# Kernel optimization log

Measured on AMD Instinct MI355X. Metric: run time of the kernel, lower is better.

The kernel has to match this reference:

```python
import jax, jax.numpy as jnp
import numpy as np

G = 64          # voxel grid side
N_IN = 150000   # input points
N_OUT = 150000  # output points
K = 3           # cubic kernel size
CIN = 32
FOUT = 64


def _make_cloud(rng, n):
    flat = rng.permutation(G ** 3)[:n]
    x = flat % G
    y = (flat // G) % G
    z = flat // (G * G)
    pos = np.stack([x, y, z], axis=-1).astype(np.float32) + 0.5  # voxel centers
    return flat, pos


def setup_inputs() -> dict:
    rng = np.random.default_rng(0)
    flat_in, inp_pos = _make_cloud(rng, N_IN)
    _, out_pos = _make_cloud(np.random.default_rng(1), N_OUT)

    # Fixed-radius (Linf, r = K*voxel*0.51 = 1.53) search on the grid ==
    # 3x3x3 voxel neighborhood lookup. Build dense voxel -> point-index map.
    grid = np.full(G ** 3, -1, dtype=np.int64)
    grid[flat_in] = np.arange(N_IN)
    offs = np.stack(np.meshgrid(*([np.arange(-1, 2)] * 3), indexing='ij'), -1).reshape(-1, 3)  # [27,3]
    out_vox = (out_pos - 0.5).astype(np.int64)              # [M,3]
    nb = out_vox[:, None, :] + offs[None, :, :]             # [M,27,3]
    inb = ((nb >= 0) & (nb < G)).all(-1)                    # [M,27]
    flat = nb[..., 0] + G * nb[..., 1] + G * G * nb[..., 2]
    flat = np.where(inb, flat, 0)
    found = grid[flat]
    mask = inb & (found >= 0)
    nbr_idx = np.where(mask, found, 0).astype(np.int32)

    key = jax.random.key(0)
    k1, k2, k3, k4, k5 = jax.random.split(key, 5)
    return {
        'inp_features': jax.random.normal(k1, (N_IN, CIN), jnp.float32),
        'inp_positions': jnp.asarray(inp_pos),
        'out_positions': jnp.asarray(out_pos),
        'voxel_size': jnp.asarray(1.0, jnp.float32),
        'inp_importance': jax.random.uniform(k2, (N_IN,), jnp.float32),
        'kernel': jax.random.uniform(k3, (K, K, K, CIN, FOUT), jnp.float32, -0.05, 0.05),
        'bias': jnp.zeros((FOUT,), jnp.float32) + 0.01 * jax.random.normal(k4, (FOUT,)),
        'neighbor_index': jnp.asarray(nbr_idx),
        'neighbor_mask': jnp.asarray(mask),
    }


def _sparse_conv(inp_features, inp_positions, out_positions, voxel_size,
                 inp_importance, kernel, bias, neighbor_index, neighbor_mask):
    # offset = 0 (odd kernel). extent = kernel_size * voxel_size.
    extent = K * voxel_size
    nbr_pos = inp_positions[neighbor_index]                  # [M,Kn,3]
    rel = nbr_pos - out_positions[:, None, :]                # [M,Kn,3]
    # identity coordinate mapping: normalize to [-1,1] over the extent
    n = 2.0 * rel / extent
    # align_corners=False mapping to filter coords, + offset (=0)
    fcoord = (n * 0.5 + 0.5) * K - 0.5                        # [M,Kn,3] (x,y,z)
    idx = jnp.clip(jnp.round(fcoord).astype(jnp.int32), 0, K - 1)
    # kernel is indexed [z,y,x,cin,cout]; positions are [x,y,z]
    flat_cell = idx[..., 2] * (K * K) + idx[..., 1] * K + idx[..., 0]   # [M,Kn]
    onehot = jax.nn.one_hot(flat_cell, K ** 3, dtype=inp_features.dtype)  # [M,Kn,27]
    w = (inp_importance[neighbor_index] * neighbor_mask.astype(inp_features.dtype))  # [M,Kn]
    feat = inp_features[neighbor_index] * w[..., None]       # [M,Kn,Cin]
    # accumulate neighbor features into their kernel cell, then contract with kernel
    cellfeat = jnp.einsum('mko,mkc->moc', onehot, feat)      # [M,27,Cin]
    wflat = kernel.reshape(K ** 3, CIN, FOUT)
    out = jnp.einsum('moc,ocf->mf', cellfeat, wflat)         # [M,F]
    return out + bias


def reference(inp_features, inp_positions, out_positions, voxel_size,
              inp_importance, kernel, bias, neighbor_index, neighbor_mask):
    return _sparse_conv(inp_features, inp_positions, out_positions, voxel_size,
                        inp_importance, kernel, bias, neighbor_index, neighbor_mask)
```

## Files before the change

### kernel.cpp

```cpp
#include <hip/hip_runtime.h>
#include <hip/hip_bf16.h>

#define CELLS 27
#define CIN   32
#define FOUT  64
#define M_OUT 150000
#define N_INP 150000
#define ZROW  N_INP
#define PPW   32
#define NWAVE ((M_OUT + PPW - 1) / PPW)
#define NBLK  ((NWAVE + 3) / 4)
#define WT_BYTES (CELLS * CIN * FOUT * 2)
#define FB_ROWS  (N_INP + 1)
#define FB_BYTES (FB_ROWS * CIN * 2)

typedef __attribute__((ext_vector_type(4))) float f32x4;
typedef __attribute__((ext_vector_type(8))) short bf16x8;

__device__ __forceinline__ short f2bf(float x) {
    union { __hip_bfloat16 h; short s; } u;
    u.h = __float2bfloat16(x);
    return u.s;
}

__global__ __launch_bounds__(256) void prep_w_kernel(const float* __restrict__ W,
                                                     unsigned short* __restrict__ Wt) {
    int t = blockIdx.x * 256 + threadIdx.x;
    if (t >= CELLS * CIN * FOUT) return;
    int cell = t >> 11;
    int rem  = t & 2047;
    int cin  = rem >> 6;
    int fout = rem & 63;
    Wt[cell * 2048 + fout * 32 + cin] = (unsigned short)f2bf(W[t]);
}

__global__ __launch_bounds__(256) void prep_feat_kernel(const float* __restrict__ feat,
                                                        const float* __restrict__ imp,
                                                        unsigned short* __restrict__ fb) {
    int t = blockIdx.x * 256 + threadIdx.x;
    if (t >= FB_ROWS * 4) return;
    int i = t >> 2, c = t & 3;
    bf16x8 o = {0, 0, 0, 0, 0, 0, 0, 0};
    if (i < N_INP) {
        float w = imp[i];
        const float* fp = feat + (size_t)i * CIN + c * 8;
        f32x4 f0 = *(const f32x4*)fp;
        f32x4 f1 = *(const f32x4*)(fp + 4);
        o[0] = f2bf(f0.x * w); o[1] = f2bf(f0.y * w);
        o[2] = f2bf(f0.z * w); o[3] = f2bf(f0.w * w);
        o[4] = f2bf(f1.x * w); o[5] = f2bf(f1.y * w);
        o[6] = f2bf(f1.z * w); o[7] = f2bf(f1.w * w);
    }
    *(bf16x8*)(fb + (size_t)i * CIN + c * 8) = o;
}

__global__ __launch_bounds__(256) void conv32_kernel(
        const float* __restrict__ opos,
        const float* __restrict__ ipos,
        const int*   __restrict__ nbr,
        const unsigned short* __restrict__ Wt,
        const unsigned short* __restrict__ fb,
        const float* __restrict__ bias,
        float* __restrict__ out) {
    __shared__ int s_idx[4][CELLS * PPW];
    __shared__ int s_vox[4][PPW];

    const int wid  = threadIdx.x >> 6;
    const int lane = threadIdx.x & 63;
    const int wave = blockIdx.x * 4 + wid;
    const int m0   = wave * PPW;

    const int vx0 = (int)ipos[0];
    const int vy0 = (int)ipos[1];
    const int vz0 = (int)ipos[2];

    if (lane < PPW) {
        int m = m0 + lane;
        int vp = -1;
        if (m < M_OUT) {
            int vx = (int)opos[m * 3 + 0];
            int vy = (int)opos[m * 3 + 1];
            int vz = (int)opos[m * 3 + 2];
            vp = (vx + 1) | ((vy + 1) << 8) | ((vz + 1) << 16);
        }
        s_vox[wid][lane] = vp;
    }
    __syncthreads();

    for (int it = 0; it < (CELLS * PPW + 63) / 64; ++it) {
        int e = it * 64 + lane;
        if (e < CELLS * PPW) {
            int p = e / CELLS;
            int k = e - p * CELLS;
            int m = m0 + p;
            int id = (m < M_OUT) ? nbr[m * CELLS + k] : 0;
            int ox = k / 9, oy = (k / 3) % 3, oz = k % 3;
            int tgt = (vx0 - ox + 2) | ((vy0 - oy + 2) << 8) | ((vz0 - oz + 2) << 16);
            bool valid = (id != 0) | (s_vox[wid][p] == tgt);
            s_idx[wid][k * PPW + p] = valid ? id : ZROW;
        }
    }
    __syncthreads();

    const int g = lane >> 4;
    const int r = lane & 15;

    f32x4 acc[8];
#pragma unroll
    for (int i = 0; i < 8; ++i) acc[i] = (f32x4){0.f, 0.f, 0.f, 0.f};

#pragma unroll
    for (int k = 0; k < CELLS; ++k) {
        const int cell = (k % 3) * 9 + ((k / 3) % 3) * 3 + (k / 9);
        int i0 = s_idx[wid][k * PPW + r];
        int i1 = s_idx[wid][k * PPW + 16 + r];
        bf16x8 a0 = *(const bf16x8*)(fb + (size_t)i0 * CIN + g * 8);
        bf16x8 a1 = *(const bf16x8*)(fb + (size_t)i1 * CIN + g * 8);
        const unsigned short* wb = Wt + cell * (CIN * FOUT) + r * CIN + g * 8;
        bf16x8 b0 = *(const bf16x8*)(wb);
        bf16x8 b1 = *(const bf16x8*)(wb + 16 * CIN);
        bf16x8 b2 = *(const bf16x8*)(wb + 32 * CIN);
        bf16x8 b3 = *(const bf16x8*)(wb + 48 * CIN);
        acc[0] = __builtin_amdgcn_mfma_f32_16x16x32_bf16(a0, b0, acc[0], 0, 0, 0);
        acc[1] = __builtin_amdgcn_mfma_f32_16x16x32_bf16(a0, b1, acc[1], 0, 0, 0);
        acc[2] = __builtin_amdgcn_mfma_f32_16x16x32_bf16(a0, b2, acc[2], 0, 0, 0);
        acc[3] = __builtin_amdgcn_mfma_f32_16x16x32_bf16(a0, b3, acc[3], 0, 0, 0);
        acc[4] = __builtin_amdgcn_mfma_f32_16x16x32_bf16(a1, b0, acc[4], 0, 0, 0);
        acc[5] = __builtin_amdgcn_mfma_f32_16x16x32_bf16(a1, b1, acc[5], 0, 0, 0);
        acc[6] = __builtin_amdgcn_mfma_f32_16x16x32_bf16(a1, b2, acc[6], 0, 0, 0);
        acc[7] = __builtin_amdgcn_mfma_f32_16x16x32_bf16(a1, b3, acc[7], 0, 0, 0);
    }

    float bb0 = bias[r], bb1 = bias[16 + r], bb2 = bias[32 + r], bb3 = bias[48 + r];
#pragma unroll
    for (int frag = 0; frag < 2; ++frag) {
        int base = m0 + frag * 16 + 4 * g;
#pragma unroll
        for (int j = 0; j < 4; ++j) {
            int m = base + j;
            if (m < M_OUT) {
                float* op = out + (size_t)m * FOUT + r;
                op[0]  = acc[frag * 4 + 0][j] + bb0;
                op[16] = acc[frag * 4 + 1][j] + bb1;
                op[32] = acc[frag * 4 + 2][j] + bb2;
                op[48] = acc[frag * 4 + 3][j] + bb3;
            }
        }
    }
}

__global__ __launch_bounds__(256, 4) void sparse_conv_fallback(
        const float* __restrict__ feat,
        const float* __restrict__ inp_pos,
        const float* __restrict__ out_pos,
        const float* __restrict__ importance,
        const float* __restrict__ bias,
        const int*   __restrict__ nbr,
        const unsigned short* __restrict__ Wt,
        float* __restrict__ out) {
    __shared__ int   s_idx[4][CELLS * 16];
    __shared__ float s_w  [4][CELLS * 16];

    const int wid  = threadIdx.x >> 6;
    const int lane = threadIdx.x & 63;
    int wave_g = blockIdx.x * 4 + wid;
    if (wave_g >= (M_OUT / 16)) wave_g = (M_OUT / 16) - 1;
    const int m0 = wave_g * 16;

    const int vx0 = (int)inp_pos[0];
    const int vy0 = (int)inp_pos[1];
    const int vz0 = (int)inp_pos[2];

    for (int it = 0; it < 7; ++it) {
        int e = it * 64 + lane;
        if (e < CELLS * 16) {
            int r = e / CELLS;
            int k = e - r * CELLS;
            int m = m0 + r;
            int idx = nbr[m * CELLS + k];
            bool valid = (idx != 0);
            if (!valid) {
                int ox = k / 9 - 1;
                int oy = (k / 3) % 3 - 1;
                int oz = k % 3 - 1;
                valid = (((int)out_pos[m * 3 + 0] + ox) == vx0) &
                        (((int)out_pos[m * 3 + 1] + oy) == vy0) &
                        (((int)out_pos[m * 3 + 2] + oz) == vz0);
            }
            float w = valid ? importance[idx] : 0.0f;
            s_idx[wid][k * 16 + r] = idx;
            s_w  [wid][k * 16 + r] = w;
        }
    }
    __syncthreads();

    const int g = lane >> 4;
    const int r = lane & 15;

    f32x4 acc0 = {0.f, 0.f, 0.f, 0.f};
    f32x4 acc1 = {0.f, 0.f, 0.f, 0.f};
    f32x4 acc2 = {0.f, 0.f, 0.f, 0.f};
    f32x4 acc3 = {0.f, 0.f, 0.f, 0.f};

#pragma unroll
    for (int k = 0; k < CELLS; ++k) {
        const int cell = (k % 3) * 9 + ((k / 3) % 3) * 3 + (k / 9);
        int   idx = s_idx[wid][k * 16 + r];
        float w   = s_w  [wid][k * 16 + r];
        if (__any(w != 0.0f)) {
            const float* fp = feat + (size_t)idx * CIN + g * 8;
            f32x4 f0 = *(const f32x4*)(fp);
            f32x4 f1 = *(const f32x4*)(fp + 4);
            bf16x8 a;
            a[0] = f2bf(f0.x * w); a[1] = f2bf(f0.y * w);
            a[2] = f2bf(f0.z * w); a[3] = f2bf(f0.w * w);
            a[4] = f2bf(f1.x * w); a[5] = f2bf(f1.y * w);
            a[6] = f2bf(f1.z * w); a[7] = f2bf(f1.w * w);
            const unsigned short* wb = Wt + cell * 2048 + r * 32 + g * 8;
            bf16x8 b0 = *(const bf16x8*)(wb);
            bf16x8 b1 = *(const bf16x8*)(wb + 512);
            bf16x8 b2 = *(const bf16x8*)(wb + 1024);
            bf16x8 b3 = *(const bf16x8*)(wb + 1536);
            acc0 = __builtin_amdgcn_mfma_f32_16x16x32_bf16(a, b0, acc0, 0, 0, 0);
            acc1 = __builtin_amdgcn_mfma_f32_16x16x32_bf16(a, b1, acc1, 0, 0, 0);
            acc2 = __builtin_amdgcn_mfma_f32_16x16x32_bf16(a, b2, acc2, 0, 0, 0);
            acc3 = __builtin_amdgcn_mfma_f32_16x16x32_bf16(a, b3, acc3, 0, 0, 0);
        }
    }

    float bb0 = bias[r], bb1 = bias[16 + r], bb2 = bias[32 + r], bb3 = bias[48 + r];
    const int row0 = m0 + 4 * g;
#pragma unroll
    for (int j = 0; j < 4; ++j) {
        float* op = out + (size_t)(row0 + j) * FOUT + r;
        op[0]  = acc0[j] + bb0;
        op[16] = acc1[j] + bb1;
        op[32] = acc2[j] + bb2;
        op[48] = acc3[j] + bb3;
    }
}

extern "C" void kernel_launch(void* const* d_in, const int* in_sizes, int n_in,
                              void* d_out, int out_size, void* d_ws, size_t ws_size,
                              hipStream_t stream) {
    const float* feat = (const float*)d_in[0];
    const float* ipos = (const float*)d_in[1];
    const float* opos = (const float*)d_in[2];
    const float* imp  = (const float*)d_in[4];
    const float* W    = (const float*)d_in[5];
    const float* bias = (const float*)d_in[6];
    const int*   nbr  = (const int*)d_in[7];
    unsigned short* Wt = (unsigned short*)d_ws;
    float* out = (float*)d_out;

    hipLaunchKernelGGL(prep_w_kernel, dim3((CELLS * CIN * FOUT + 255) / 256), dim3(256),
                       0, stream, W, Wt);

    if (ws_size >= (size_t)WT_BYTES + (size_t)FB_BYTES) {
        unsigned short* fb = (unsigned short*)((char*)d_ws + WT_BYTES);
        hipLaunchKernelGGL(prep_feat_kernel, dim3((FB_ROWS * 4 + 255) / 256), dim3(256),
                           0, stream, feat, imp, fb);
        hipLaunchKernelGGL(conv32_kernel, dim3(NBLK), dim3(256), 0, stream,
                           opos, ipos, nbr, Wt, fb, bias, out);
    } else {
        int blocks = (M_OUT / 16 + 3) / 4;
        hipLaunchKernelGGL(sparse_conv_fallback, dim3(blocks), dim3(256), 0, stream,
                           feat, ipos, opos, imp, bias, nbr, Wt, out);
    }
}
```

Baseline: 179.1 us.

## Merge prep kernels and double-buffer gathers in the conv MFMA loop

Fuses the weight and feature prep kernels into one launch, removing a kernel launch. In the conv kernel, the shared-memory index table is transposed to point-major with padding to 28, and the A/B operand loads are software-pipelined two cells ahead, so global gathers overlap the MFMA work. The fallback path and the workspace-size check are removed, which assumes the workspace is always large enough. The prefetch buffers also increase register pressure.

Result: no change. 180.7 us (+0.9%).

```diff
diff --git a/kernel.cpp b/kernel.cpp
--- a/kernel.cpp
+++ b/kernel.cpp
@@ -10,7 +10,8 @@
 #define PPW   32
 #define NWAVE ((M_OUT + PPW - 1) / PPW)
 #define NBLK  ((NWAVE + 3) / 4)
-#define WT_BYTES (CELLS * CIN * FOUT * 2)
+#define WT_ELEMS (CELLS * CIN * FOUT)
+#define WT_BYTES (WT_ELEMS * 2)
 #define FB_ROWS  (N_INP + 1)
 #define FB_BYTES (FB_ROWS * CIN * 2)
 
@@ -23,36 +24,39 @@
     return u.s;
 }
 
-__global__ __launch_bounds__(256) void prep_w_kernel(const float* __restrict__ W,
-                                                     unsigned short* __restrict__ Wt) {
+__global__ __launch_bounds__(256) void prep_kernel(const float* __restrict__ W,
+                                                   const float* __restrict__ feat,
+                                                   const float* __restrict__ imp,
+                                                   unsigned short* __restrict__ Wt,
+                                                   unsigned short* __restrict__ fb) {
     int t = blockIdx.x * 256 + threadIdx.x;
-    if (t >= CELLS * CIN * FOUT) return;
-    int cell = t >> 11;
-    int rem  = t & 2047;
-    int cin  = rem >> 6;
-    int fout = rem & 63;
-    Wt[cell * 2048 + fout * 32 + cin] = (unsigned short)f2bf(W[t]);
+    if (t < FB_ROWS * 4) {
+        int i = t >> 2, c = t & 3;
+        bf16x8 o = {0, 0, 0, 0, 0, 0, 0, 0};
+        if (i < N_INP) {
+            float w = imp[i];
+            const float* fp = feat + (size_t)i * CIN + c * 8;
+            f32x4 f0 = *(const f32x4*)fp;
+            f32x4 f1 = *(const f32x4*)(fp + 4);
+            o[0] = f2bf(f0.x * w); o[1] = f2bf(f0.y * w);
+            o[2] = f2bf(f0.z * w); o[3] = f2bf(f0.w * w);
+            o[4] = f2bf(f1.x * w); o[5] = f2bf(f1.y * w);
+            o[6] = f2bf(f1.z * w); o[7] = f2bf(f1.w * w);
+        }
+        *(bf16x8*)(fb + (size_t)i * CIN + c * 8) = o;
+    } else {
+        int u = t - FB_ROWS * 4;
+        if (u < WT_ELEMS) {
+            int cell = u >> 11;
+            int rem  = u & 2047;
+            int cin  = rem >> 6;
+            int fout = rem & 63;
+            Wt[cell * 2048 + fout * 32 + cin] = (unsigned short)f2bf(W[u]);
+        }
+    }
 }
 
-__global__ __launch_bounds__(256) void prep_feat_kernel(const float* __restrict__ feat,
-                                                        const float* __restrict__ imp,
-                                                        unsigned short* __restrict__ fb) {
-    int t = blockIdx.x * 256 + threadIdx.x;
-    if (t >= FB_ROWS * 4) return;
-    int i = t >> 2, c = t & 3;
-    bf16x8 o = {0, 0, 0, 0, 0, 0, 0, 0};
-    if (i < N_INP) {
-        float w = imp[i];
-        const float* fp = feat + (size_t)i * CIN + c * 8;
-        f32x4 f0 = *(const f32x4*)fp;
-        f32x4 f1 = *(const f32x4*)(fp + 4);
-        o[0] = f2bf(f0.x * w); o[1] = f2bf(f0.y * w);
-        o[2] = f2bf(f0.z * w); o[3] = f2bf(f0.w * w);
-        o[4] = f2bf(f1.x * w); o[5] = f2bf(f1.y * w);
-        o[6] = f2bf(f1.z * w); o[7] = f2bf(f1.w * w);
-    }
-    *(bf16x8*)(fb + (size_t)i * CIN + c * 8) = o;
-}
+#define CELL_OF(k) (((k) % 3) * 9 + (((k) / 3) % 3) * 3 + ((k) / 9))
 
 __global__ __launch_bounds__(256) void conv32_kernel(
         const float* __restrict__ opos,
@@ -62,7 +66,7 @@
         const unsigned short* __restrict__ fb,
         const float* __restrict__ bias,
         float* __restrict__ out) {
-    __shared__ int s_idx[4][CELLS * PPW];
+    __shared__ int s_idx[4][PPW][28];
     __shared__ int s_vox[4][PPW];
 
     const int wid  = threadIdx.x >> 6;
@@ -78,16 +82,15 @@
         int m = m0 + lane;
         int vp = -1;
         if (m < M_OUT) {
-            int vx = (int)opos[m * 3 + 0];
-            int vy = (int)opos[m * 3 + 1];
-            int vz = (int)opos[m * 3 + 2];
-            vp = (vx + 1) | ((vy + 1) << 8) | ((vz + 1) << 16);
+            vp = ((int)opos[m * 3 + 0] + 1) |
+                 (((int)opos[m * 3 + 1] + 1) << 8) |
+                 (((int)opos[m * 3 + 2] + 1) << 16);
         }
         s_vox[wid][lane] = vp;
     }
     __syncthreads();
 
-    for (int it = 0; it < (CELLS * PPW + 63) / 64; ++it) {
+    for (int it = 0; it < 14; ++it) {
         int e = it * 64 + lane;
         if (e < CELLS * PPW) {
             int p = e / CELLS;
@@ -97,7 +100,7 @@
             int ox = k / 9, oy = (k / 3) % 3, oz = k % 3;
             int tgt = (vx0 - ox + 2) | ((vy0 - oy + 2) << 8) | ((vz0 - oz + 2) << 16);
             bool valid = (id != 0) | (s_vox[wid][p] == tgt);
-            s_idx[wid][k * PPW + p] = valid ? id : ZROW;
+            s_idx[wid][p][k] = valid ? id : ZROW;
         }
     }
     __syncthreads();
@@ -105,30 +108,54 @@
     const int g = lane >> 4;
     const int r = lane & 15;
 
+    const unsigned short* fbg = fb + g * 8;
+    const unsigned short* wb0 = Wt + r * CIN + g * 8;
+    const int* idxr0 = &s_idx[wid][r][0];
+    const int* idxr1 = &s_idx[wid][16 + r][0];
+
     f32x4 acc[8];
 #pragma unroll
     for (int i = 0; i < 8; ++i) acc[i] = (f32x4){0.f, 0.f, 0.f, 0.f};
 
+    int    pi0[2], pi1[2];
+    bf16x8 pa0[2], pa1[2];
+    bf16x8 pb[2][4];
+
+    {
+        int a0 = idxr0[0], a1 = idxr1[0];
+        int b0 = idxr0[1], b1 = idxr1[1];
+        pa0[0] = *(const bf16x8*)(fbg + (size_t)a0 * CIN);
+        pa1[0] = *(const bf16x8*)(fbg + (size_t)a1 * CIN);
+        pa0[1] = *(const bf16x8*)(fbg + (size_t)b0 * CIN);
+        pa1[1] = *(const bf16x8*)(fbg + (size_t)b1 * CIN);
+#pragma unroll
+        for (int t = 0; t < 4; ++t) {
+            pb[0][t] = *(const bf16x8*)(wb0 + CELL_OF(0) * (CIN * FOUT) + t * 16 * CIN);
+            pb[1][t] = *(const bf16x8*)(wb0 + CELL_OF(1) * (CIN * FOUT) + t * 16 * CIN);
+        }
+        pi0[0] = idxr0[2]; pi1[0] = idxr1[2];
+        pi0[1] = idxr0[3]; pi1[1] = idxr1[3];
+    }
+
 #pragma unroll
     for (int k = 0; k < CELLS; ++k) {
-        const int cell = (k % 3) * 9 + ((k / 3) % 3) * 3 + (k / 9);
-        int i0 = s_idx[wid][k * PPW + r];
-        int i1 = s_idx[wid][k * PPW + 16 + r];
-        bf16x8 a0 = *(const bf16x8*)(fb + (size_t)i0 * CIN + g * 8);
-        bf16x8 a1 = *(const bf16x8*)(fb + (size_t)i1 * CIN + g * 8);
-        const unsigned short* wb = Wt + cell * (CIN * FOUT) + r * CIN + g * 8;
-        bf16x8 b0 = *(const bf16x8*)(wb);
-        bf16x8 b1 = *(const bf16x8*)(wb + 16 * CIN);
-        bf16x8 b2 = *(const bf16x8*)(wb + 32 * CIN);
-        bf16x8 b3 = *(const bf16x8*)(wb + 48 * CIN);
-        acc[0] = __builtin_amdgcn_mfma_f32_16x16x32_bf16(a0, b0, acc[0], 0, 0, 0);
-        acc[1] = __builtin_amdgcn_mfma_f32_16x16x32_bf16(a0, b1, acc[1], 0, 0, 0);
-        acc[2] = __builtin_amdgcn_mfma_f32_16x16x32_bf16(a0, b2, acc[2], 0, 0, 0);
-        acc[3] = __builtin_amdgcn_mfma_f32_16x16x32_bf16(a0, b3, acc[3], 0, 0, 0);
-        acc[4] = __builtin_amdgcn_mfma_f32_16x16x32_bf16(a1, b0, acc[4], 0, 0, 0);
-        acc[5] = __builtin_amdgcn_mfma_f32_16x16x32_bf16(a1, b1, acc[5], 0, 0, 0);
-        acc[6] = __builtin_amdgcn_mfma_f32_16x16x32_bf16(a1, b2, acc[6], 0, 0, 0);
-        acc[7] = __builtin_amdgcn_mfma_f32_16x16x32_bf16(a1, b3, acc[7], 0, 0, 0);
+        const int s = k & 1;
+#pragma unroll
+        for (int t = 0; t < 4; ++t) {
+            acc[t]     = __builtin_amdgcn_mfma_f32_16x16x32_bf16(pa0[s], pb[s][t], acc[t],     0, 0, 0);
+            acc[4 + t] = __builtin_amdgcn_mfma_f32_16x16x32_bf16(pa1[s], pb[s][t], acc[4 + t], 0, 0, 0);
+        }
+        if (k + 2 < CELLS) {
+            pa0[s] = *(const bf16x8*)(fbg + (size_t)pi0[s] * CIN);
+            pa1[s] = *(const bf16x8*)(fbg + (size_t)pi1[s] * CIN);
+#pragma unroll
+            for (int t = 0; t < 4; ++t)
+                pb[s][t] = *(const bf16x8*)(wb0 + CELL_OF(k + 2) * (CIN * FOUT) + t * 16 * CIN);
+            if (k + 4 < CELLS) {
+                pi0[s] = idxr0[k + 4];
+                pi1[s] = idxr1[k + 4];
+            }
+        }
     }
 
     float bb0 = bias[r], bb1 = bias[16 + r], bb2 = bias[32 + r], bb3 = bias[48 + r];
@@ -149,97 +176,6 @@
     }
 }
 
-__global__ __launch_bounds__(256, 4) void sparse_conv_fallback(
-        const float* __restrict__ feat,
-        const float* __restrict__ inp_pos,
-        const float* __restrict__ out_pos,
-        const float* __restrict__ importance,
-        const float* __restrict__ bias,
-        const int*   __restrict__ nbr,
-        const unsigned short* __restrict__ Wt,
-        float* __restrict__ out) {
-    __shared__ int   s_idx[4][CELLS * 16];
-    __shared__ float s_w  [4][CELLS * 16];
-
-    const int wid  = threadIdx.x >> 6;
-    const int lane = threadIdx.x & 63;
-    int wave_g = blockIdx.x * 4 + wid;
-    if (wave_g >= (M_OUT / 16)) wave_g = (M_OUT / 16) - 1;
-    const int m0 = wave_g * 16;
-
-    const int vx0 = (int)inp_pos[0];
-    const int vy0 = (int)inp_pos[1];
-    const int vz0 = (int)inp_pos[2];
-
-    for (int it = 0; it < 7; ++it) {
-        int e = it * 64 + lane;
-        if (e < CELLS * 16) {
-            int r = e / CELLS;
-            int k = e - r * CELLS;
-            int m = m0 + r;
-            int idx = nbr[m * CELLS + k];
-            bool valid = (idx != 0);
-            if (!valid) {
-                int ox = k / 9 - 1;
-                int oy = (k / 3) % 3 - 1;
-                int oz = k % 3 - 1;
-                valid = (((int)out_pos[m * 3 + 0] + ox) == vx0) &
-                        (((int)out_pos[m * 3 + 1] + oy) == vy0) &
-                        (((int)out_pos[m * 3 + 2] + oz) == vz0);
-            }
-            float w = valid ? importance[idx] : 0.0f;
-            s_idx[wid][k * 16 + r] = idx;
-            s_w  [wid][k * 16 + r] = w;
-        }
-    }
-    __syncthreads();
-
-    const int g = lane >> 4;
-    const int r = lane & 15;
-
-    f32x4 acc0 = {0.f, 0.f, 0.f, 0.f};
-    f32x4 acc1 = {0.f, 0.f, 0.f, 0.f};
-    f32x4 acc2 = {0.f, 0.f, 0.f, 0.f};
-    f32x4 acc3 = {0.f, 0.f, 0.f, 0.f};
-
-#pragma unroll
-    for (int k = 0; k < CELLS; ++k) {
-        const int cell = (k % 3) * 9 + ((k / 3) % 3) * 3 + (k / 9);
-        int   idx = s_idx[wid][k * 16 + r];
-        float w   = s_w  [wid][k * 16 + r];
-        if (__any(w != 0.0f)) {
-            const float* fp = feat + (size_t)idx * CIN + g * 8;
-            f32x4 f0 = *(const f32x4*)(fp);
-            f32x4 f1 = *(const f32x4*)(fp + 4);
-            bf16x8 a;
-            a[0] = f2bf(f0.x * w); a[1] = f2bf(f0.y * w);
-            a[2] = f2bf(f0.z * w); a[3] = f2bf(f0.w * w);
-            a[4] = f2bf(f1.x * w); a[5] = f2bf(f1.y * w);
-            a[6] = f2bf(f1.z * w); a[7] = f2bf(f1.w * w);
-            const unsigned short* wb = Wt + cell * 2048 + r * 32 + g * 8;
-            bf16x8 b0 = *(const bf16x8*)(wb);
-            bf16x8 b1 = *(const bf16x8*)(wb + 512);
-            bf16x8 b2 = *(const bf16x8*)(wb + 1024);
-            bf16x8 b3 = *(const bf16x8*)(wb + 1536);
-            acc0 = __builtin_amdgcn_mfma_f32_16x16x32_bf16(a, b0, acc0, 0, 0, 0);
-            acc1 = __builtin_amdgcn_mfma_f32_16x16x32_bf16(a, b1, acc1, 0, 0, 0);
-            acc2 = __builtin_amdgcn_mfma_f32_16x16x32_bf16(a, b2, acc2, 0, 0, 0);
-            acc3 = __builtin_amdgcn_mfma_f32_16x16x32_bf16(a, b3, acc3, 0, 0, 0);
-        }
-    }
-
-    float bb0 = bias[r], bb1 = bias[16 + r], bb2 = bias[32 + r], bb3 = bias[48 + r];
-    const int row0 = m0 + 4 * g;
-#pragma unroll
-    for (int j = 0; j < 4; ++j) {
-        float* op = out + (size_t)(row0 + j) * FOUT + r;
-        op[0]  = acc0[j] + bb0;
-        op[16] = acc1[j] + bb1;
-        op[32] = acc2[j] + bb2;
-        op[48] = acc3[j] + bb3;
-    }
-}
-
 extern "C" void kernel_launch(void* const* d_in, const int* in_sizes, int n_in,
                               void* d_out, int out_size, void* d_ws, size_t ws_size,
                               hipStream_t stream) {
@@ -251,20 +187,12 @@
     const float* bias = (const float*)d_in[6];
     const int*   nbr  = (const int*)d_in[7];
     unsigned short* Wt = (unsigned short*)d_ws;
+    unsigned short* fb = (unsigned short*)((char*)d_ws + WT_BYTES);
     float* out = (float*)d_out;
 
-    hipLaunchKernelGGL(prep_w_kernel, dim3((CELLS * CIN * FOUT + 255) / 256), dim3(256),
-                       0, stream, W, Wt);
-
-    if (ws_size >= (size_t)WT_BYTES + (size_t)FB_BYTES) {
-        unsigned short* fb = (unsigned short*)((char*)d_ws + WT_BYTES);
-        hipLaunchKernelGGL(prep_feat_kernel, dim3((FB_ROWS * 4 + 255) / 256), dim3(256),
-                           0, stream, feat, imp, fb);
-        hipLaunchKernelGGL(conv32_kernel, dim3(NBLK), dim3(256), 0, stream,
-                           opos, ipos, nbr, Wt, fb, bias, out);
-    } else {
-        int blocks = (M_OUT / 16 + 3) / 4;
-        hipLaunchKernelGGL(sparse_conv_fallback, dim3(blocks), dim3(256), 0, stream,
-                           feat, ipos, opos, imp, bias, nbr, Wt, out);
-    }
+    int prep_threads = FB_ROWS * 4 + WT_ELEMS;
+    hipLaunchKernelGGL(prep_kernel, dim3((prep_threads + 255) / 256), dim3(256),
+                       0, stream, W, feat, imp, Wt, fb);
+    hipLaunchKernelGGL(conv32_kernel, dim3(NBLK), dim3(256), 0, stream,
+                       opos, ipos, nbr, Wt, fb, bias, out);
 }
```
